# Performance work log

Measured on AMD Instinct MI355X. Metric: run time of the kernel, lower is better.

## Reference

```python
import jax, jax.numpy as jnp
import numpy as np

N = 50000
E = 800000
IN_C = 128
HID = 64
HEADS = 4
OUT_C = 64


def setup_inputs() -> dict:
    key = jax.random.key(0)
    ks = jax.random.split(key, 20)
    s = 0.05
    inp = {
        "x": jax.random.normal(ks[0], (N, IN_C), dtype=jnp.float32),
        "edge_index": jax.random.randint(ks[1], (2, E), 0, N, dtype=jnp.int64),
        # layer 0: in=128 -> heads=4, C=64
        "W0": jax.random.normal(ks[2], (IN_C, HEADS * HID), jnp.float32) * s,
        "a0s": jax.random.normal(ks[3], (HEADS, HID), jnp.float32) * s,
        "a0d": jax.random.normal(ks[4], (HEADS, HID), jnp.float32) * s,
        "b0": jnp.zeros((HEADS * HID,), jnp.float32),
        # layer 1: 256 -> heads=4, C=64
        "W1": jax.random.normal(ks[5], (HEADS * HID, HEADS * HID), jnp.float32) * s,
        "a1s": jax.random.normal(ks[6], (HEADS, HID), jnp.float32) * s,
        "a1d": jax.random.normal(ks[7], (HEADS, HID), jnp.float32) * s,
        "b1": jnp.zeros((HEADS * HID,), jnp.float32),
        # layer 2: 256 -> heads=1, C=64
        "W2": jax.random.normal(ks[8], (HEADS * HID, HID), jnp.float32) * s,
        "a2s": jax.random.normal(ks[9], (1, HID), jnp.float32) * s,
        "a2d": jax.random.normal(ks[10], (1, HID), jnp.float32) * s,
        "b2": jnp.zeros((HID,), jnp.float32),
        # prediction head: Linear(64 -> 64)
        "hw": jax.random.normal(ks[11], (HID, OUT_C), jnp.float32) * s,
        "hb": jnp.zeros((OUT_C,), jnp.float32),
    }
    return inp


def gat_conv(x, src, dst, W, a_s, a_d, b, heads, n_nodes):
    # x: [N, F_in]; returns [N, heads*C]
    C = a_s.shape[1]
    h = (x @ W).reshape(n_nodes, heads, C)          # [N,H,C]
    alpha_s = jnp.sum(h * a_s, axis=-1)             # [N,H]
    alpha_d = jnp.sum(h * a_d, axis=-1)             # [N,H]
    e = jax.nn.leaky_relu(alpha_s[src] + alpha_d[dst], negative_slope=0.2)  # [E,H]
    m = jax.ops.segment_max(e, dst, num_segments=n_nodes)                  # per-dst max
    ex = jnp.exp(e - m[dst])
    denom = jax.ops.segment_sum(ex, dst, num_segments=n_nodes)
    alpha = ex / (denom[dst] + 1e-16)               # [E,H]
    out = jax.ops.segment_sum(alpha[:, :, None] * h[src], dst, num_segments=n_nodes)
    return out.reshape(n_nodes, heads * C) + b


def reference(x, edge_index, W0, a0s, a0d, b0, W1, a1s, a1d, b1, W2, a2s, a2d, b2, hw, hb):
    n = x.shape[0]
    # PyG GATConv default add_self_loops=True
    loop = jnp.arange(n, dtype=edge_index.dtype)
    src = jnp.concatenate([edge_index[0], loop])
    dst = jnp.concatenate([edge_index[1], loop])

    h = gat_conv(x, src, dst, W0, a0s, a0d, b0, HEADS, n)
    h = jax.nn.relu(h)
    h = gat_conv(h, src, dst, W1, a1s, a1d, b1, HEADS, n)
    h = jax.nn.relu(h)
    h = gat_conv(h, src, dst, W2, a2s, a2d, b2, 1, n)
    # batch is None -> mean over all nodes, keepdim
    g = jnp.mean(h, axis=0, keepdims=True)          # [1, HID]
    return g @ hw + hb                               # [1, OUT_C]
```

## Files before the change

### kernel.cpp

```cpp
#include <hip/hip_runtime.h>
#include <hip/hip_bf16.h>
#include <cstddef>

#define NN 50000
#define EE 800000
#define NB ((NN + 255) / 256)

typedef __attribute__((ext_vector_type(8))) short short8;
typedef __attribute__((ext_vector_type(4))) float f32x4;

#define GLB __attribute__((address_space(1)))
#define LDS __attribute__((address_space(3)))

__device__ __forceinline__ float leaky(float x) { return x >= 0.f ? x : 0.2f * x; }
__device__ __forceinline__ float bf2f(unsigned short u) {
  return __uint_as_float(((unsigned int)u) << 16);
}
__device__ __forceinline__ float bflo(unsigned int v) { return __uint_as_float(v << 16); }
__device__ __forceinline__ float bfhi(unsigned int v) { return __uint_as_float(v & 0xFFFF0000u); }
__device__ __forceinline__ unsigned short f2bf(float f) {
  __hip_bfloat16 b = __float2bfloat16(f);
  return __builtin_bit_cast(unsigned short, b);
}
__device__ __forceinline__ float selh(float4 v, int h) {
  float a = (h & 1) ? v.y : v.x;
  float b = (h & 1) ? v.w : v.z;
  return (h & 2) ? b : a;
}
__device__ __forceinline__ void accum8(float a, uint4 v, float* acc) {
  acc[0] += a * bflo(v.x); acc[1] += a * bfhi(v.x);
  acc[2] += a * bflo(v.y); acc[3] += a * bfhi(v.y);
  acc[4] += a * bflo(v.z); acc[5] += a * bfhi(v.z);
  acc[6] += a * bflo(v.w); acc[7] += a * bfhi(v.w);
}

__global__ __launch_bounds__(256) void gemm_bf16_k(const unsigned short* __restrict__ A,
                                                   const unsigned short* __restrict__ Bt,
                                                   unsigned short* __restrict__ Cb,
                                                   int K, int Nfull,
                                                   const float* __restrict__ a_s,
                                                   const float* __restrict__ a_d,
                                                   float* __restrict__ als,
                                                   float* __restrict__ ald,
                                                   float* __restrict__ selfex) {
  __shared__ __align__(16) unsigned short As[128 * 32];
  __shared__ __align__(16) unsigned short Bs[64 * 32];
  const int tid = threadIdx.x;
  const int lane = tid & 63;
  const int w = tid >> 6;
  const int bm = blockIdx.x * 128;
  const int bn = blockIdx.y * 64;
  const int quad = lane >> 4;
  const int l16 = lane & 15;
  const int lrow = lane >> 2;
  const int lseg = lane & 3;
  f32x4 acc[2][4] = {};
  for (int kc = 0; kc < K; kc += 32) {
#pragma unroll
    for (int c = 0; c < 2; ++c) {
      int row = w * 32 + c * 16 + lrow;
      int g = lseg ^ ((row >> 2) & 3);
      int sr = bm + row; if (sr >= NN) sr = NN - 1;
      const unsigned short* gp = A + (size_t)sr * K + kc + g * 8;
      __builtin_amdgcn_global_load_lds((const GLB void*)gp,
                                       (LDS void*)&As[(w * 32 + c * 16) * 32], 16, 0, 0);
    }
    {
      int row = w * 16 + lrow;
      int g = lseg ^ ((row >> 2) & 3);
      const unsigned short* gp = Bt + (size_t)(bn + row) * K + kc + g * 8;
      __builtin_amdgcn_global_load_lds((const GLB void*)gp,
                                       (LDS void*)&Bs[(w * 16) * 32], 16, 0, 0);
    }
    __syncthreads();
    const int ra0 = w * 32 + l16;
    const int ra1 = ra0 + 16;
    short8 afr0 = *(const short8*)&As[ra0 * 32 + ((quad ^ ((ra0 >> 2) & 3)) << 3)];
    short8 afr1 = *(const short8*)&As[ra1 * 32 + ((quad ^ ((ra1 >> 2) & 3)) << 3)];
#pragma unroll
    for (int nt = 0; nt < 4; ++nt) {
      int rb = nt * 16 + l16;
      short8 bfr = *(const short8*)&Bs[rb * 32 + ((quad ^ ((rb >> 2) & 3)) << 3)];
      acc[0][nt] = __builtin_amdgcn_mfma_f32_16x16x32_bf16(afr0, bfr, acc[0][nt], 0, 0, 0);
      acc[1][nt] = __builtin_amdgcn_mfma_f32_16x16x32_bf16(afr1, bfr, acc[1][nt], 0, 0, 0);
    }
    __syncthreads();
  }
  const int head = bn >> 6;
  const int Hmul = Nfull >> 6;
  float vs[2][4] = {};
  float vd[2][4] = {};
#pragma unroll
  for (int nt = 0; nt < 4; ++nt) {
    const float asv = a_s[head * 64 + nt * 16 + l16];
    const float adv = a_d[head * 64 + nt * 16 + l16];
#pragma unroll
    for (int mt = 0; mt < 2; ++mt)
#pragma unroll
      for (int reg = 0; reg < 4; ++reg) {
        unsigned short c = f2bf(acc[mt][nt][reg]);
        int r = bm + w * 32 + mt * 16 + quad * 4 + reg;
        if (r < NN) Cb[(size_t)r * Nfull + bn + nt * 16 + l16] = c;
        float hv = bf2f(c);
        vs[mt][reg] += hv * asv;
        vd[mt][reg] += hv * adv;
      }
  }
#pragma unroll
  for (int off = 1; off < 16; off <<= 1) {
#pragma unroll
    for (int mt = 0; mt < 2; ++mt)
#pragma unroll
      for (int reg = 0; reg < 4; ++reg) {
        vs[mt][reg] += __shfl_xor(vs[mt][reg], off, 64);
        vd[mt][reg] += __shfl_xor(vd[mt][reg], off, 64);
      }
  }
  if (l16 == 0) {
#pragma unroll
    for (int mt = 0; mt < 2; ++mt)
#pragma unroll
      for (int reg = 0; reg < 4; ++reg) {
        int r = bm + w * 32 + mt * 16 + quad * 4 + reg;
        if (r < NN) {
          als[(size_t)r * Hmul + head] = vs[mt][reg];
          ald[(size_t)r * Hmul + head] = vd[mt][reg];
          selfex[(size_t)r * Hmul + head] = __expf(leaky(vs[mt][reg] + vd[mt][reg]));
        }
      }
  }
}

__global__ __launch_bounds__(256) void hist_k(const int* __restrict__ ei, int* deg) {
  int i = blockIdx.x * 256 + threadIdx.x;
  if (i < EE) atomicAdd(&deg[ei[EE + i]], 1);
}

__global__ __launch_bounds__(256) void scan1_k(const int* __restrict__ deg,
                                               int* __restrict__ incl,
                                               int* __restrict__ partial) {
  __shared__ int s[256];
  int t = threadIdx.x;
  int i = blockIdx.x * 256 + t;
  int v = (i < NN) ? deg[i] : 0;
  s[t] = v;
  __syncthreads();
  for (int off = 1; off < 256; off <<= 1) {
    int u = (t >= off) ? s[t - off] : 0;
    __syncthreads();
    s[t] += u;
    __syncthreads();
  }
  if (i < NN) incl[i] = s[t];
  if (t == 255) partial[blockIdx.x] = s[255];
}

__global__ __launch_bounds__(256) void scan23_k(const int* __restrict__ deg,
                                                const int* __restrict__ incl,
                                                const int* __restrict__ partial,
                                                int* __restrict__ rowptr,
                                                int* __restrict__ cursor) {
  __shared__ int s[256];
  __shared__ int ex[256];
  int t = threadIdx.x;
  int v = (t < NB) ? partial[t] : 0;
  s[t] = v;
  __syncthreads();
  for (int off = 1; off < 256; off <<= 1) {
    int u = (t >= off) ? s[t - off] : 0;
    __syncthreads();
    s[t] += u;
    __syncthreads();
  }
  ex[t] = s[t] - v;
  __syncthreads();
  int base = ex[blockIdx.x];
  int i = blockIdx.x * 256 + t;
  if (i < NN) {
    int r = base + incl[i] - deg[i];
    rowptr[i] = r;
    cursor[i] = r;
  }
}

__global__ __launch_bounds__(256) void scatter_k(const int* __restrict__ ei,
                                                 int* __restrict__ cursor,
                                                 int* __restrict__ csr_src) {
  int i = blockIdx.x * 256 + threadIdx.x;
  if (i >= EE) return;
  int d = ei[EE + i];
  int p = atomicAdd(&cursor[d], 1);
  csr_src[p] = ei[i];
}

__global__ __launch_bounds__(256) void aggr4c_k(const int* __restrict__ rowptr,
                                                const int* __restrict__ deg,
                                                const int* __restrict__ csr_src,
                                                const float* __restrict__ als,
                                                const float* __restrict__ ald,
                                                const float* __restrict__ selfex,
                                                const uint4* __restrict__ hb4,
                                                const float* __restrict__ bias,
                                                uint4* __restrict__ out4) {
  const int dst = blockIdx.x * 4 + (threadIdx.x >> 6);
  const int lane = threadIdx.x & 63;
  const int slot = lane >> 4;
  const int l16 = lane & 15;
  const int head = l16 >> 2;
  const int rs = rowptr[dst];
  const int dg = deg[dst];
  const float aldv = ald[dst * 4 + head];

  float acc[16] = {};
  float dsum = 0.f;
  if (slot == 0) {
    float a = selfex[dst * 4 + head];
    dsum += a;
    uint4 v0 = hb4[(size_t)dst * 32 + l16 * 2];
    uint4 v1 = hb4[(size_t)dst * 32 + l16 * 2 + 1];
    accum8(a, v0, acc);
    accum8(a, v1, acc + 8);
  }
  int j = slot;
  for (; j + 4 < dg; j += 8) {
    int s0 = csr_src[rs + j];
    int s1 = csr_src[rs + j + 4];
    float e0 = als[s0 * 4 + head];
    float e1 = als[s1 * 4 + head];
    uint4 va0 = hb4[(size_t)s0 * 32 + l16 * 2];
    uint4 vb0 = hb4[(size_t)s0 * 32 + l16 * 2 + 1];
    uint4 va1 = hb4[(size_t)s1 * 32 + l16 * 2];
    uint4 vb1 = hb4[(size_t)s1 * 32 + l16 * 2 + 1];
    float a0 = __expf(leaky(e0 + aldv));
    float a1 = __expf(leaky(e1 + aldv));
    dsum += a0 + a1;
    accum8(a0, va0, acc);
    accum8(a0, vb0, acc + 8);
    accum8(a1, va1, acc);
    accum8(a1, vb1, acc + 8);
  }
  for (; j < dg; j += 4) {
    int s0 = csr_src[rs + j];
    float e0 = als[s0 * 4 + head];
    uint4 va0 = hb4[(size_t)s0 * 32 + l16 * 2];
    uint4 vb0 = hb4[(size_t)s0 * 32 + l16 * 2 + 1];
    float a0 = __expf(leaky(e0 + aldv));
    dsum += a0;
    accum8(a0, va0, acc);
    accum8(a0, vb0, acc + 8);
  }
#pragma unroll
  for (int k = 0; k < 16; ++k) {
    acc[k] += __shfl_xor(acc[k], 16, 64);
    acc[k] += __shfl_xor(acc[k], 32, 64);
  }
  dsum += __shfl_xor(dsum, 16, 64);
  dsum += __shfl_xor(dsum, 32, 64);
  if (slot == 0) {
    const float inv = 1.f / (dsum + 1e-16f);
    const float* bz = bias + l16 * 16;
    uint4 o0, o1;
    float c0, c1;
    c0 = fmaxf(acc[0] * inv + bz[0], 0.f);   c1 = fmaxf(acc[1] * inv + bz[1], 0.f);
    o0.x = ((unsigned int)f2bf(c1) << 16) | f2bf(c0);
    c0 = fmaxf(acc[2] * inv + bz[2], 0.f);   c1 = fmaxf(acc[3] * inv + bz[3], 0.f);
    o0.y = ((unsigned int)f2bf(c1) << 16) | f2bf(c0);
    c0 = fmaxf(acc[4] * inv + bz[4], 0.f);   c1 = fmaxf(acc[5] * inv + bz[5], 0.f);
    o0.z = ((unsigned int)f2bf(c1) << 16) | f2bf(c0);
    c0 = fmaxf(acc[6] * inv + bz[6], 0.f);   c1 = fmaxf(acc[7] * inv + bz[7], 0.f);
    o0.w = ((unsigned int)f2bf(c1) << 16) | f2bf(c0);
    c0 = fmaxf(acc[8] * inv + bz[8], 0.f);   c1 = fmaxf(acc[9] * inv + bz[9], 0.f);
    o1.x = ((unsigned int)f2bf(c1) << 16) | f2bf(c0);
    c0 = fmaxf(acc[10] * inv + bz[10], 0.f); c1 = fmaxf(acc[11] * inv + bz[11], 0.f);
    o1.y = ((unsigned int)f2bf(c1) << 16) | f2bf(c0);
    c0 = fmaxf(acc[12] * inv + bz[12], 0.f); c1 = fmaxf(acc[13] * inv + bz[13], 0.f);
    o1.z = ((unsigned int)f2bf(c1) << 16) | f2bf(c0);
    c0 = fmaxf(acc[14] * inv + bz[14], 0.f); c1 = fmaxf(acc[15] * inv + bz[15], 0.f);
    o1.w = ((unsigned int)f2bf(c1) << 16) | f2bf(c0);
    out4[(size_t)dst * 32 + l16 * 2] = o0;
    out4[(size_t)dst * 32 + l16 * 2 + 1] = o1;
  }
}

__global__ __launch_bounds__(256) void aggr1c_k(const int* __restrict__ rowptr,
                                                const int* __restrict__ deg,
                                                const int* __restrict__ csr_src,
                                                const float* __restrict__ als,
                                                const float* __restrict__ ald,
                                                const float* __restrict__ selfex,
                                                const uint4* __restrict__ hb4,
                                                const float* __restrict__ bias,
                                                float* __restrict__ out) {
  const int dst = blockIdx.x * 4 + (threadIdx.x >> 6);
  const int lane = threadIdx.x & 63;
  const int slot = lane >> 3;
  const int c8 = lane & 7;
  const int rs = rowptr[dst];
  const int dg = deg[dst];
  const float aldv = ald[dst];

  float acc[8] = {};
  float dsum = 0.f;
  if (slot == 0) {
    float a = selfex[dst];
    dsum += a;
    uint4 v = hb4[(size_t)dst * 8 + c8];
    accum8(a, v, acc);
  }
  for (int j = slot; j < dg; j += 8) {
    int s = csr_src[rs + j];
    float e = als[s];
    uint4 v = hb4[(size_t)s * 8 + c8];
    float a = __expf(leaky(e + aldv));
    dsum += a;
    accum8(a, v, acc);
  }
#pragma unroll
  for (int k = 0; k < 8; ++k) {
    acc[k] += __shfl_xor(acc[k], 8, 64);
    acc[k] += __shfl_xor(acc[k], 16, 64);
    acc[k] += __shfl_xor(acc[k], 32, 64);
  }
  dsum += __shfl_xor(dsum, 8, 64);
  dsum += __shfl_xor(dsum, 16, 64);
  dsum += __shfl_xor(dsum, 32, 64);
  if (slot == 0) {
    const float inv = 1.f / (dsum + 1e-16f);
    const float4 bz0 = *(const float4*)(bias + c8 * 8);
    const float4 bz1 = *(const float4*)(bias + c8 * 8 + 4);
    float4 o0 = make_float4(acc[0] * inv + bz0.x, acc[1] * inv + bz0.y,
                            acc[2] * inv + bz0.z, acc[3] * inv + bz0.w);
    float4 o1 = make_float4(acc[4] * inv + bz1.x, acc[5] * inv + bz1.y,
                            acc[6] * inv + bz1.z, acc[7] * inv + bz1.w);
    *(float4*)(out + (size_t)dst * 64 + c8 * 8) = o0;
    *(float4*)(out + (size_t)dst * 64 + c8 * 8 + 4) = o1;
  }
}

__global__ __launch_bounds__(256) void prep_k(const float2* __restrict__ x2,
                                              unsigned int* __restrict__ xb_u,
                                              const float* __restrict__ W0,
                                              unsigned short* __restrict__ W0t,
                                              const float* __restrict__ W1,
                                              unsigned short* __restrict__ W1t,
                                              const float* __restrict__ W2,
                                              unsigned short* __restrict__ W2t,
                                              int* __restrict__ deg,
                                              float* __restrict__ g) {
  int bid = blockIdx.x;
  int tid = threadIdx.x;
  if (bid < 12500) {
    int i = bid * 256 + tid;
    float2 v = x2[i];
    xb_u[i] = ((unsigned int)f2bf(v.y) << 16) | f2bf(v.x);
    return;
  }
  if (bid < 12948) {
    int r = (bid - 12500) * 256 + tid;
    if (r < 32768) {
      int n = r >> 7, k = r & 127;
      W0t[n * 128 + k] = f2bf(W0[k * 256 + n]);
    } else if (r < 98304) {
      int rr = r - 32768;
      int n = rr >> 8, k = rr & 255;
      W1t[n * 256 + k] = f2bf(W1[k * 256 + n]);
    } else {
      int rr = r - 98304;
      int n = rr >> 8, k = rr & 255;
      W2t[n * 256 + k] = f2bf(W2[k * 64 + n]);
    }
    return;
  }
  if (bid < 13144) {
    int i = (bid - 12948) * 256 + tid;
    if (i < NN) deg[i] = 0;
    return;
  }
  if (tid < 68) g[tid] = 0.f;
}

__global__ __launch_bounds__(256) void colsum_head_k(const float* __restrict__ h2,
                                                     float* __restrict__ g,
                                                     unsigned int* __restrict__ cnt,
                                                     const float* __restrict__ hw,
                                                     const float* __restrict__ hb,
                                                     float* __restrict__ out) {
  __shared__ float s[256];
  __shared__ float sg[64];
  __shared__ unsigned int sdone;
  int tid = threadIdx.x;
  int c = tid & 63, rg = tid >> 6;
  float acc = 0.f;
  for (int n = blockIdx.x * 4 + rg; n < NN; n += gridDim.x * 4)
    acc += h2[n * 64 + c];
  s[tid] = acc;
  __syncthreads();
  if (tid < 64) atomicAdd(&g[c], s[c] + s[64 + c] + s[128 + c] + s[192 + c]);
  __threadfence();
  __syncthreads();
  if (tid == 0) sdone = atomicAdd(cnt, 1);
  __syncthreads();
  if (sdone != gridDim.x - 1) return;
  if (tid < 64) sg[tid] = atomicAdd(&g[tid], 0.f);
  __syncthreads();
  if (tid < 64) {
    const float invN = 1.0f / (float)NN;
    float a2 = hb[tid];
#pragma unroll 8
    for (int cc = 0; cc < 64; ++cc) a2 += sg[cc] * invN * hw[cc * 64 + tid];
    out[tid] = a2;
  }
}

extern "C" void kernel_launch(void* const* d_in, const int* in_sizes, int n_in,
                              void* d_out, int out_size, void* d_ws, size_t ws_size,
                              hipStream_t stream) {
  const float* x   = (const float*)d_in[0];
  const int*   ei  = (const int*)d_in[1];
  const float* W0  = (const float*)d_in[2];
  const float* a0s = (const float*)d_in[3];
  const float* a0d = (const float*)d_in[4];
  const float* b0  = (const float*)d_in[5];
  const float* W1  = (const float*)d_in[6];
  const float* a1s = (const float*)d_in[7];
  const float* a1d = (const float*)d_in[8];
  const float* b1  = (const float*)d_in[9];
  const float* W2  = (const float*)d_in[10];
  const float* a2s = (const float*)d_in[11];
  const float* a2d = (const float*)d_in[12];
  const float* b2  = (const float*)d_in[13];
  const float* hw  = (const float*)d_in[14];
  const float* hb  = (const float*)d_in[15];
  float* out = (float*)d_out;

  char* w = (char*)d_ws;
  unsigned short* xb   = (unsigned short*)w; w += (size_t)NN * 128 * 2;
  unsigned short* bufG = (unsigned short*)w; w += (size_t)NN * 256 * 2;
  unsigned short* bufA = (unsigned short*)w; w += (size_t)NN * 256 * 2;
  float* bufF = (float*)w;                   w += (size_t)NN * 64 * 4;
  unsigned short* W0t = (unsigned short*)w;  w += 256 * 128 * 2;
  unsigned short* W1t = (unsigned short*)w;  w += 256 * 256 * 2;
  unsigned short* W2t = (unsigned short*)w;  w += 64 * 256 * 2;
  float* als  = (float*)w;    w += (size_t)NN * 4 * 4;
  float* ald  = (float*)w;    w += (size_t)NN * 4 * 4;
  float* sfx  = (float*)w;    w += (size_t)NN * 4 * 4;
  int* deg     = (int*)w;     w += (size_t)NN * 4;
  int* rowptr  = (int*)w;     w += (size_t)NN * 4;
  int* cursor  = (int*)w;     w += (size_t)NN * 4;
  int* incl    = (int*)w;     w += (size_t)NN * 4;
  int* partial = (int*)w;     w += 256 * 4;
  int* csr_src = (int*)w;     w += (size_t)EE * 4;
  float* g    = (float*)w;    w += 256;

  prep_k<<<13145, 256, 0, stream>>>((const float2*)x, (unsigned int*)xb,
                                    W0, W0t, W1, W1t, W2, W2t, deg, g);

  hist_k<<<(EE + 255) / 256, 256, 0, stream>>>(ei, deg);
  scan1_k<<<NB, 256, 0, stream>>>(deg, incl, partial);
  scan23_k<<<NB, 256, 0, stream>>>(deg, incl, partial, rowptr, cursor);
  scatter_k<<<(EE + 255) / 256, 256, 0, stream>>>(ei, cursor, csr_src);

  const int GX = (NN + 127) / 128;
  const int GA = NN / 4;

  auto layer4 = [&](const unsigned short* in, int K, const unsigned short* Wt,
                    const float* a_s, const float* a_d, const float* bias,
                    unsigned short* hbuf, unsigned short* obuf) {
    gemm_bf16_k<<<dim3(GX, 4), 256, 0, stream>>>(in, Wt, hbuf, K, 256,
                                                 a_s, a_d, als, ald, sfx);
    aggr4c_k<<<GA, 256, 0, stream>>>(rowptr, deg, csr_src, als, ald, sfx,
                                     (const uint4*)hbuf, bias, (uint4*)obuf);
  };

  layer4(xb, 128, W0t, a0s, a0d, b0, bufG, bufA);
  layer4(bufA, 256, W1t, a1s, a1d, b1, bufG, bufA);

  gemm_bf16_k<<<dim3(GX, 1), 256, 0, stream>>>(bufA, W2t, bufG, 256, 64,
                                               a2s, a2d, als, ald, sfx);
  aggr1c_k<<<GA, 256, 0, stream>>>(rowptr, deg, csr_src, als, ald, sfx,
                                   (const uint4*)bufG, b2, bufF);

  colsum_head_k<<<256, 256, 0, stream>>>(bufF, g, (unsigned int*)(g + 64), hw, hb, out);
}
```

Measured before the change: 437.5 us.

## Split 4-head aggregation across blocks, one head per block

The multi-head GAT aggregation kernel now launches four times as many blocks, each handling one head for four destination nodes. Each wave uses 8 edge slots of 8 lanes, and each lane loads one 16-byte chunk instead of two, which halves per-thread accumulators and raises parallelism and occupancy. The cost is that csr_src, rowptr and deg are read four times per destination, the per-block work is smaller, and the 2x edge unrolling is dropped.

```diff
diff --git a/kernel.cpp b/kernel.cpp
--- a/kernel.cpp
+++ b/kernel.cpp
@@ -21,11 +21,6 @@
 __device__ __forceinline__ unsigned short f2bf(float f) {
   __hip_bfloat16 b = __float2bfloat16(f);
   return __builtin_bit_cast(unsigned short, b);
-}
-__device__ __forceinline__ float selh(float4 v, int h) {
-  float a = (h & 1) ? v.y : v.x;
-  float b = (h & 1) ? v.w : v.z;
-  return (h & 2) ? b : a;
 }
 __device__ __forceinline__ void accum8(float a, uint4 v, float* acc) {
   acc[0] += a * bflo(v.x); acc[1] += a * bfhi(v.x);
@@ -193,7 +188,7 @@
   csr_src[p] = ei[i];
 }
 
-__global__ __launch_bounds__(256) void aggr4c_k(const int* __restrict__ rowptr,
+__global__ __launch_bounds__(256) void aggr4s_k(const int* __restrict__ rowptr,
                                                 const int* __restrict__ deg,
                                                 const int* __restrict__ csr_src,
                                                 const float* __restrict__ als,
@@ -202,83 +197,56 @@
                                                 const uint4* __restrict__ hb4,
                                                 const float* __restrict__ bias,
                                                 uint4* __restrict__ out4) {
-  const int dst = blockIdx.x * 4 + (threadIdx.x >> 6);
+  const int sl = blockIdx.x & 3;
+  const int grp = blockIdx.x >> 2;
+  const int dst = grp * 4 + (threadIdx.x >> 6);
   const int lane = threadIdx.x & 63;
-  const int slot = lane >> 4;
-  const int l16 = lane & 15;
-  const int head = l16 >> 2;
+  const int slot = lane >> 3;
+  const int c8 = lane & 7;
   const int rs = rowptr[dst];
   const int dg = deg[dst];
-  const float aldv = ald[dst * 4 + head];
-
-  float acc[16] = {};
+  const float aldv = ald[dst * 4 + sl];
+
+  float acc[8] = {};
   float dsum = 0.f;
   if (slot == 0) {
-    float a = selfex[dst * 4 + head];
+    float a = selfex[dst * 4 + sl];
     dsum += a;
-    uint4 v0 = hb4[(size_t)dst * 32 + l16 * 2];
-    uint4 v1 = hb4[(size_t)dst * 32 + l16 * 2 + 1];
-    accum8(a, v0, acc);
-    accum8(a, v1, acc + 8);
-  }
-  int j = slot;
-  for (; j + 4 < dg; j += 8) {
-    int s0 = csr_src[rs + j];
-    int s1 = csr_src[rs + j + 4];
-    float e0 = als[s0 * 4 + head];
-    float e1 = als[s1 * 4 + head];
-    uint4 va0 = hb4[(size_t)s0 * 32 + l16 * 2];
-    uint4 vb0 = hb4[(size_t)s0 * 32 + l16 * 2 + 1];
-    uint4 va1 = hb4[(size_t)s1 * 32 + l16 * 2];
-    uint4 vb1 = hb4[(size_t)s1 * 32 + l16 * 2 + 1];
-    float a0 = __expf(leaky(e0 + aldv));
-    float a1 = __expf(leaky(e1 + aldv));
-    dsum += a0 + a1;
-    accum8(a0, va0, acc);
-    accum8(a0, vb0, acc + 8);
-    accum8(a1, va1, acc);
-    accum8(a1, vb1, acc + 8);
-  }
-  for (; j < dg; j += 4) {
-    int s0 = csr_src[rs + j];
-    float e0 = als[s0 * 4 + head];
-    uint4 va0 = hb4[(size_t)s0 * 32 + l16 * 2];
-    uint4 vb0 = hb4[(size_t)s0 * 32 + l16 * 2 + 1];
-    float a0 = __expf(leaky(e0 + aldv));
-    dsum += a0;
-    accum8(a0, va0, acc);
-    accum8(a0, vb0, acc + 8);
-  }
-#pragma unroll
-  for (int k = 0; k < 16; ++k) {
+    uint4 v = hb4[(size_t)dst * 32 + sl * 8 + c8];
+    accum8(a, v, acc);
+  }
+  for (int j = slot; j < dg; j += 8) {
+    int s = csr_src[rs + j];
+    float e = als[s * 4 + sl];
+    uint4 v = hb4[(size_t)s * 32 + sl * 8 + c8];
+    float a = __expf(leaky(e + aldv));
+    dsum += a;
+    accum8(a, v, acc);
+  }
+#pragma unroll
+  for (int k = 0; k < 8; ++k) {
+    acc[k] += __shfl_xor(acc[k], 8, 64);
     acc[k] += __shfl_xor(acc[k], 16, 64);
     acc[k] += __shfl_xor(acc[k], 32, 64);
   }
+  dsum += __shfl_xor(dsum, 8, 64);
   dsum += __shfl_xor(dsum, 16, 64);
   dsum += __shfl_xor(dsum, 32, 64);
   if (slot == 0) {
     const float inv = 1.f / (dsum + 1e-16f);
-    const float* bz = bias + l16 * 16;
-    uint4 o0, o1;
+    const float4 bz0 = *(const float4*)(bias + sl * 64 + c8 * 8);
+    const float4 bz1 = *(const float4*)(bias + sl * 64 + c8 * 8 + 4);
     float c0, c1;
-    c0 = fmaxf(acc[0] * inv + bz[0], 0.f);   c1 = fmaxf(acc[1] * inv + bz[1], 0.f);
-    o0.x = ((unsigned int)f2bf(c1) << 16) | f2bf(c0);
-    c0 = fmaxf(acc[2] * inv + bz[2], 0.f);   c1 = fmaxf(acc[3] * inv + bz[3], 0.f);
-    o0.y = ((unsigned int)f2bf(c1) << 16) | f2bf(c0);
-    c0 = fmaxf(acc[4] * inv + bz[4], 0.f);   c1 = fmaxf(acc[5] * inv + bz[5], 0.f);
-    o0.z = ((unsigned int)f2bf(c1) << 16) | f2bf(c0);
-    c0 = fmaxf(acc[6] * inv + bz[6], 0.f);   c1 = fmaxf(acc[7] * inv + bz[7], 0.f);
-    o0.w = ((unsigned int)f2bf(c1) << 16) | f2bf(c0);
-    c0 = fmaxf(acc[8] * inv + bz[8], 0.f);   c1 = fmaxf(acc[9] * inv + bz[9], 0.f);
-    o1.x = ((unsigned int)f2bf(c1) << 16) | f2bf(c0);
-    c0 = fmaxf(acc[10] * inv + bz[10], 0.f); c1 = fmaxf(acc[11] * inv + bz[11], 0.f);
-    o1.y = ((unsigned int)f2bf(c1) << 16) | f2bf(c0);
-    c0 = fmaxf(acc[12] * inv + bz[12], 0.f); c1 = fmaxf(acc[13] * inv + bz[13], 0.f);
-    o1.z = ((unsigned int)f2bf(c1) << 16) | f2bf(c0);
-    c0 = fmaxf(acc[14] * inv + bz[14], 0.f); c1 = fmaxf(acc[15] * inv + bz[15], 0.f);
-    o1.w = ((unsigned int)f2bf(c1) << 16) | f2bf(c0);
-    out4[(size_t)dst * 32 + l16 * 2] = o0;
-    out4[(size_t)dst * 32 + l16 * 2 + 1] = o1;
+    uint4 o;
+    c0 = fmaxf(acc[0] * inv + bz0.x, 0.f); c1 = fmaxf(acc[1] * inv + bz0.y, 0.f);
+    o.x = ((unsigned int)f2bf(c1) << 16) | f2bf(c0);
+    c0 = fmaxf(acc[2] * inv + bz0.z, 0.f); c1 = fmaxf(acc[3] * inv + bz0.w, 0.f);
+    o.y = ((unsigned int)f2bf(c1) << 16) | f2bf(c0);
+    c0 = fmaxf(acc[4] * inv + bz1.x, 0.f); c1 = fmaxf(acc[5] * inv + bz1.y, 0.f);
+    o.z = ((unsigned int)f2bf(c1) << 16) | f2bf(c0);
+    c0 = fmaxf(acc[6] * inv + bz1.z, 0.f); c1 = fmaxf(acc[7] * inv + bz1.w, 0.f);
+    o.w = ((unsigned int)f2bf(c1) << 16) | f2bf(c0);
+    out4[(size_t)dst * 32 + sl * 8 + c8] = o;
   }
 }
 
@@ -462,14 +430,15 @@
 
   const int GX = (NN + 127) / 128;
   const int GA = NN / 4;
+  const int GA4 = GA * 4;
 
   auto layer4 = [&](const unsigned short* in, int K, const unsigned short* Wt,
                     const float* a_s, const float* a_d, const float* bias,
                     unsigned short* hbuf, unsigned short* obuf) {
     gemm_bf16_k<<<dim3(GX, 4), 256, 0, stream>>>(in, Wt, hbuf, K, 256,
                                                  a_s, a_d, als, ald, sfx);
-    aggr4c_k<<<GA, 256, 0, stream>>>(rowptr, deg, csr_src, als, ald, sfx,
-                                     (const uint4*)hbuf, bias, (uint4*)obuf);
+    aggr4s_k<<<GA4, 256, 0, stream>>>(rowptr, deg, csr_src, als, ald, sfx,
+                                      (const uint4*)hbuf, bias, (uint4*)obuf);
   };
 
   layer4(xb, 128, W0t, a0s, a0d, b0, bufG, bufA);
```

Result: slower. 498.3 us (+13.9%).
